# Performance work log

Hardware: AMD Instinct MI355X
Metric: run time of the kernel (lower is better)

## Reference

```python
import jax, jax.numpy as jnp
import numpy as np

N_HEAD, QK_DIM, V_DIM = 8, 32, 32
INNER = N_HEAD * V_DIM  # 256
D_MODEL = 256
N_VAR = 2
NEG = -1e9
LN_EPS = 1e-5


def irregular_rope(q, t):
    # q: [BN, L, H, D], t: [BN, L]
    D = q.shape[-1]
    inv_freq = 1.0 / (10000.0 ** (jnp.arange(0, D, 2, dtype=jnp.float32) / D))  # [D/2]
    ang = t[:, :, None, None] * inv_freq[None, None, None, :]  # [BN, L, 1, D/2]
    cos, sin = jnp.cos(ang), jnp.sin(ang)
    q1, q2 = q[..., 0::2], q[..., 1::2]
    out = jnp.stack([q1 * cos - q2 * sin, q1 * sin + q2 * cos], axis=-1)
    return out.reshape(q.shape)


def layernorm(x, g, b):
    mu = jnp.mean(x, axis=-1, keepdims=True)
    var = jnp.mean((x - mu) ** 2, axis=-1, keepdims=True)
    return (x - mu) * jax.lax.rsqrt(var + LN_EPS) * g + b


def setup_inputs() -> dict:
    key = jax.random.key(0)
    ks = jax.random.split(key, 14)
    B, PN, PL = 16, 64, 128
    x = jax.random.normal(ks[0], (B, PN, PL, N_VAR), dtype=jnp.float32)
    t = jnp.sort(jax.random.uniform(ks[1], (B, PN, PL + 1), dtype=jnp.float32) * 100.0, axis=-1)
    mask = jax.random.randint(ks[2], (B, PN, PL + 1), 0, 2, dtype=jnp.int32)
    mask = mask.at[..., 0].set(1)  # emb token never masked
    s = 0.05
    return {
        "x": x, "t": t, "mask": mask,
        "emb_token": jnp.zeros((1, 1, 1, N_VAR), dtype=jnp.float32),
        "Wq": jax.random.normal(ks[3], (N_VAR, N_HEAD * QK_DIM), dtype=jnp.float32) * s,
        "Wk": jax.random.normal(ks[4], (N_VAR, N_HEAD * QK_DIM), dtype=jnp.float32) * s,
        "Wv": jax.random.normal(ks[5], (N_VAR, N_HEAD * V_DIM), dtype=jnp.float32) * s,
        "Wo": jax.random.normal(ks[6], (INNER, D_MODEL), dtype=jnp.float32) * s,
        "ln_g": jnp.ones((INNER,), dtype=jnp.float32),
        "ln_b": jnp.zeros((INNER,), dtype=jnp.float32),
        "W1": jax.random.normal(ks[7], (INNER, 4 * INNER), dtype=jnp.float32) * s,
        "b1": jnp.zeros((4 * INNER,), dtype=jnp.float32),
        "W2": jax.random.normal(ks[8], (4 * INNER, INNER), dtype=jnp.float32) * s,
        "b2": jnp.zeros((INNER,), dtype=jnp.float32),
    }


def reference(x, t, mask, emb_token, Wq, Wk, Wv, Wo, ln_g, ln_b, W1, b1, W2, b2):
    B, PN, PL, _ = x.shape
    L = PL + 1
    BN = B * PN
    emb = jnp.broadcast_to(emb_token, (B, PN, 1, N_VAR))
    _x = jnp.concatenate([emb, x], axis=2)  # [B, PN, L, 2]
    Q = (_x @ Wq).reshape(BN, L, N_HEAD, QK_DIM)
    K = (_x @ Wk).reshape(BN, L, N_HEAD, QK_DIM)
    V = (_x @ Wv).reshape(BN, L, N_HEAD, V_DIM)
    tt = t.reshape(BN, L)
    Q = irregular_rope(Q, tt)
    K = irregular_rope(K, tt)
    # attention: [BN, H, L, L]
    scores = jnp.einsum('blhd,bmhd->bhlm', Q, K) / jnp.sqrt(jnp.float32(QK_DIM))
    m = mask.reshape(BN, L).astype(jnp.float32)
    mask_mat = (m[:, :, None] * m[:, None, :])[:, None, :, :]  # [BN,1,L,L]
    scores = jnp.where(mask_mat > 0, scores, NEG)
    attn = jax.nn.softmax(scores, axis=-1)
    ctx = jnp.einsum('bhlm,bmhd->blhd', attn, V)  # [BN, L, H, Dv]
    last = ctx[:, 0].reshape(B, PN, INNER)  # emb-token output
    h = layernorm(last, ln_g, ln_b)
    h = jax.nn.relu(h @ W1 + b1) @ W2 + b2
    last = last + h
    return last @ Wo  # [B, PN, D_MODEL]
```

## Files before the change

kernel.cpp:

```cpp
#include <hip/hip_runtime.h>
#include <math.h>

#define LSEQ   129
#define PLEN   128
#define NHEAD  8
#define DHEAD  32
#define INNER  256
#define HID    1024

typedef _Float16 h2 __attribute__((ext_vector_type(2)));

__device__ __forceinline__ float dot2(h2 a, h2 b, float c) {
#if __has_builtin(__builtin_amdgcn_fdot2)
    return __builtin_amdgcn_fdot2(a, b, c, false);
#else
    return c + (float)a.x * (float)b.x + (float)a.y * (float)b.y;
#endif
}

__device__ __forceinline__ h2 pack2(float a, float b) {
    h2 v; v.x = (_Float16)a; v.y = (_Float16)b; return v;
}

__global__ __launch_bounds__(256) void convert_kernel(
    const float* __restrict__ W1, const float* __restrict__ W2,
    const float* __restrict__ Wo,
    h2* __restrict__ W1p, h2* __restrict__ W2p, h2* __restrict__ Wop)
{
    int idx = blockIdx.x * 256 + threadIdx.x;
    if (idx < 131072) {
        int c2 = idx >> 10, jc = idx & 1023;
        W1p[idx] = pack2(W1[(2 * c2) * HID + jc], W1[(2 * c2 + 1) * HID + jc]);
    } else if (idx < 262144) {
        int l = idx - 131072;
        int c2 = l >> 8, jc = l & 255;
        W2p[l] = pack2(W2[(2 * c2) * INNER + jc], W2[(2 * c2 + 1) * INNER + jc]);
    } else if (idx < 294912) {
        int l = idx - 262144;
        int c2 = l >> 8, jc = l & 255;
        Wop[l] = pack2(Wo[(2 * c2) * INNER + jc], Wo[(2 * c2 + 1) * INNER + jc]);
    }
}

__global__ __launch_bounds__(256) void attn_kernel(
    const float* __restrict__ x,
    const float* __restrict__ t,
    const int*   __restrict__ mask,
    const float* __restrict__ emb,
    const float* __restrict__ Wq,
    const float* __restrict__ Wk,
    const float* __restrict__ Wv,
    float*       __restrict__ last)
{
    const int bn  = blockIdx.x;
    const int tid = threadIdx.x;

    __shared__ float2 cs_s[16][132];
    __shared__ float2 x_s[132];
    __shared__ float4 ab_s[8][16];
    __shared__ float  sc_s[8][132];
    __shared__ int    mask_s[132];
    __shared__ float  hstat_s[8][3];

    const float* tb = t + bn * LSEQ;
    const float t0  = tb[0];
    const float e0 = emb[0], e1 = emb[1];

    if (tid < 130) {
        float2 v;
        if (tid == 0)       v = make_float2(e0, e1);
        else if (tid <= 128) v = ((const float2*)(x + bn * PLEN * 2))[tid - 1];
        else                 v = make_float2(0.f, 0.f);
        x_s[tid] = v;
    }
    if (tid < 129) mask_s[tid] = mask[bn * LSEQ + tid];

    for (int i = tid; i < 129 * 16; i += 256) {
        int m = i >> 4, j = i & 15;
        float invf = exp2f(-(float)j * 0.8304820237218407f);
        float sv, cv;
        __sincosf((tb[m] - t0) * invf, &sv, &cv);
        cs_s[j][m] = make_float2(cv, sv);
    }

    if (tid < 128) {
        int h = tid >> 4, j = tid & 15;
        int ce = h * 32 + 2 * j, co = ce + 1;
        float qe = e0 * Wq[ce] + e1 * Wq[256 + ce];
        float qo = e0 * Wq[co] + e1 * Wq[256 + co];
        float k0e = Wk[ce], k0o = Wk[co];
        float k1e = Wk[256 + ce], k1o = Wk[256 + co];
        const float sc = 0.17677669529663687f;
        ab_s[h][j] = make_float4((qe * k0e + qo * k0o) * sc,
                                 (qo * k0e - qe * k0o) * sc,
                                 (qe * k1e + qo * k1o) * sc,
                                 (qo * k1e - qe * k1o) * sc);
    }
    __syncthreads();

    const int lane = tid & 63;
    const int wv   = tid >> 6;
    const int h    = wv * 2 + (lane >> 5);
    const int l32  = lane & 31;

    float4 ab[16];
#pragma unroll
    for (int j = 0; j < 16; ++j) ab[j] = ab_s[h][j];

#pragma unroll
    for (int k = 0; k < 5; ++k) {
        int m = l32 + 32 * k;
        if (m < 129) {
            float2 xv = x_s[m];
            float accA = 0.f, accB = 0.f;
#pragma unroll
            for (int j = 0; j < 16; ++j) {
                float2 cs = cs_s[j][m];
                accA = fmaf(cs.x, ab[j].x, accA);
                accA = fmaf(cs.y, ab[j].y, accA);
                accB = fmaf(cs.x, ab[j].z, accB);
                accB = fmaf(cs.y, ab[j].w, accB);
            }
            sc_s[h][m] = accA * xv.x + accB * xv.y;
        }
    }
    __syncthreads();

    const int mask0 = mask_s[0];
    float se[5];
    float M = -1e30f;
#pragma unroll
    for (int k = 0; k < 5; ++k) {
        int m = l32 + 32 * k;
        float s;
        if (m < 129) {
            s = sc_s[h][m];
            if (mask0 == 0)          s = 0.f;
            else if (mask_s[m] == 0) s = -1e9f;
        } else s = -1e30f;
        se[k] = s;
        M = fmaxf(M, s);
    }
#pragma unroll
    for (int off = 16; off >= 1; off >>= 1) M = fmaxf(M, __shfl_xor(M, off, 64));

    float den = 0.f, S0 = 0.f, S1 = 0.f;
#pragma unroll
    for (int k = 0; k < 5; ++k) {
        int m = l32 + 32 * k;
        if (m < 129) {
            float e = __expf(se[k] - M);
            float2 xv = x_s[m];
            den += e;
            S0 = fmaf(e, xv.x, S0);
            S1 = fmaf(e, xv.y, S1);
        }
    }
#pragma unroll
    for (int off = 16; off >= 1; off >>= 1) {
        den += __shfl_xor(den, off, 64);
        S0  += __shfl_xor(S0,  off, 64);
        S1  += __shfl_xor(S1,  off, 64);
    }
    if (l32 == 0) {
        hstat_s[h][0] = den; hstat_s[h][1] = S0; hstat_s[h][2] = S1;
    }
    __syncthreads();

    {
        int hh = tid >> 5;
        float inv = 1.f / hstat_s[hh][0];
        last[bn * 256 + tid] =
            (hstat_s[hh][1] * Wv[tid] + hstat_s[hh][2] * Wv[256 + tid]) * inv;
    }
}

__global__ __launch_bounds__(1024) void mlp_kernel(
    const float* __restrict__ last,
    const float* __restrict__ ln_g,
    const float* __restrict__ ln_b,
    const h2*    __restrict__ W1p,
    const float* __restrict__ b1,
    const h2*    __restrict__ W2p,
    const float* __restrict__ b2,
    const h2*    __restrict__ Wop,
    float*       __restrict__ out)
{
    const int tid = threadIdx.x;
    const int r0  = blockIdx.x * 4;
    const int rg  = tid >> 8;
    const int ch  = tid & 255;

    __shared__ float x_s[4][INNER];
    __shared__ h2    h2_s[4][128];
    __shared__ h2    y2_s[4][512];
    __shared__ float p_s[4][4][INNER];
    __shared__ h2    r2_s[4][128];
    __shared__ float red_s[16][2];

    float xv = last[(r0 + rg) * INNER + ch];
    x_s[rg][ch] = xv;

    float s1 = xv, s2 = xv * xv;
#pragma unroll
    for (int off = 32; off >= 1; off >>= 1) {
        s1 += __shfl_xor(s1, off, 64);
        s2 += __shfl_xor(s2, off, 64);
    }
    const int wave = tid >> 6;
    if ((tid & 63) == 0) { red_s[wave][0] = s1; red_s[wave][1] = s2; }
    __syncthreads();

    {
        float t1 = red_s[4 * rg + 0][0] + red_s[4 * rg + 1][0] +
                   red_s[4 * rg + 2][0] + red_s[4 * rg + 3][0];
        float t2 = red_s[4 * rg + 0][1] + red_s[4 * rg + 1][1] +
                   red_s[4 * rg + 2][1] + red_s[4 * rg + 3][1];
        float mu  = t1 * (1.f / 256.f);
        float var = t2 * (1.f / 256.f) - mu * mu;
        float rs  = rsqrtf(var + 1e-5f);
        float hv  = (xv - mu) * rs * ln_g[ch] + ln_b[ch];
        float ho  = __shfl_xor(hv, 1, 64);
        if ((ch & 1) == 0) h2_s[rg][ch >> 1] = pack2(hv, ho);
    }
    __syncthreads();

    {
        float a0, a1v, a2v, a3;
        a0 = a1v = a2v = a3 = b1[tid];
        const h2* w = W1p + tid;
#pragma unroll 16
        for (int c2 = 0; c2 < 128; ++c2) {
            h2 wv = w[c2 * HID];
            a0  = dot2(h2_s[0][c2], wv, a0);
            a1v = dot2(h2_s[1][c2], wv, a1v);
            a2v = dot2(h2_s[2][c2], wv, a2v);
            a3  = dot2(h2_s[3][c2], wv, a3);
        }
        a0 = fmaxf(a0, 0.f); a1v = fmaxf(a1v, 0.f);
        a2v = fmaxf(a2v, 0.f); a3 = fmaxf(a3, 0.f);
        float o0 = __shfl_xor(a0, 1, 64);
        float o1 = __shfl_xor(a1v, 1, 64);
        float o2 = __shfl_xor(a2v, 1, 64);
        float o3 = __shfl_xor(a3, 1, 64);
        if ((tid & 1) == 0) {
            int p = tid >> 1;
            y2_s[0][p] = pack2(a0, o0);
            y2_s[1][p] = pack2(a1v, o1);
            y2_s[2][p] = pack2(a2v, o2);
            y2_s[3][p] = pack2(a3, o3);
        }
    }
    __syncthreads();

    {
        float a0 = 0.f, a1v = 0.f, a2v = 0.f, a3 = 0.f;
        const h2* w = W2p + rg * 128 * INNER + ch;
#pragma unroll 16
        for (int i = 0; i < 128; ++i) {
            h2 wv = w[i * INNER];
            int c2 = rg * 128 + i;
            a0  = dot2(y2_s[0][c2], wv, a0);
            a1v = dot2(y2_s[1][c2], wv, a1v);
            a2v = dot2(y2_s[2][c2], wv, a2v);
            a3  = dot2(y2_s[3][c2], wv, a3);
        }
        p_s[rg][0][ch] = a0;
        p_s[rg][1][ch] = a1v;
        p_s[rg][2][ch] = a2v;
        p_s[rg][3][ch] = a3;
    }
    __syncthreads();

    {
        float rv = x_s[rg][ch] + b2[ch] +
                   p_s[0][rg][ch] + p_s[1][rg][ch] +
                   p_s[2][rg][ch] + p_s[3][rg][ch];
        float ro = __shfl_xor(rv, 1, 64);
        if ((ch & 1) == 0) r2_s[rg][ch >> 1] = pack2(rv, ro);
    }
    __syncthreads();

    {
        float a0 = 0.f, a1v = 0.f, a2v = 0.f, a3 = 0.f;
        const h2* w = Wop + rg * 32 * INNER + ch;
#pragma unroll
        for (int i = 0; i < 32; ++i) {
            h2 wv = w[i * INNER];
            int c2 = rg * 32 + i;
            a0  = dot2(r2_s[0][c2], wv, a0);
            a1v = dot2(r2_s[1][c2], wv, a1v);
            a2v = dot2(r2_s[2][c2], wv, a2v);
            a3  = dot2(r2_s[3][c2], wv, a3);
        }
        p_s[rg][0][ch] = a0;
        p_s[rg][1][ch] = a1v;
        p_s[rg][2][ch] = a2v;
        p_s[rg][3][ch] = a3;
    }
    __syncthreads();

    out[(r0 + rg) * INNER + ch] = p_s[0][rg][ch] + p_s[1][rg][ch] +
                                  p_s[2][rg][ch] + p_s[3][rg][ch];
}

extern "C" void kernel_launch(void* const* d_in, const int* in_sizes, int n_in,
                              void* d_out, int out_size, void* d_ws, size_t ws_size,
                              hipStream_t stream) {
    const float* x    = (const float*)d_in[0];
    const float* t    = (const float*)d_in[1];
    const int*   mask = (const int*)  d_in[2];
    const float* emb  = (const float*)d_in[3];
    const float* Wq   = (const float*)d_in[4];
    const float* Wk   = (const float*)d_in[5];
    const float* Wv   = (const float*)d_in[6];
    const float* Wo   = (const float*)d_in[7];
    const float* ln_g = (const float*)d_in[8];
    const float* ln_b = (const float*)d_in[9];
    const float* W1   = (const float*)d_in[10];
    const float* b1   = (const float*)d_in[11];
    const float* W2   = (const float*)d_in[12];
    const float* b2   = (const float*)d_in[13];
    float* out = (float*)d_out;

    const int BN = in_sizes[1] / LSEQ;

    char* ws = (char*)d_ws;
    float* last_ws = (float*)ws;
    h2* W1p = (h2*)(ws + (1u << 20));
    h2* W2p = (h2*)(ws + (1u << 20) + (512u << 10));
    h2* Wop = (h2*)(ws + (2u << 20));

    convert_kernel<<<1152, 256, 0, stream>>>(W1, W2, Wo, W1p, W2p, Wop);
    attn_kernel<<<BN, 256, 0, stream>>>(x, t, mask, emb, Wq, Wk, Wv, last_ws);
    mlp_kernel<<<BN / 4, 1024, 0, stream>>>(last_ws, ln_g, ln_b, W1p, b1,
                                            W2p, b2, Wop, out);
}
```

Measured before the change: 111.8 us.

## Fuse weight fp16 conversion into attention kernel and use 8-wide packed weights

Removes the separate convert kernel launch by having each attention block convert a slice of W1/W2/Wo to fp16 before its attention work. The packed format changes from pairs to groups of 8 halves, so the MLP kernel issues 128-bit weight loads and 128-bit LDS reads with four dot2 ops each, instead of 32-bit loads. Activations are stored as plain fp16 arrays in shared memory without the shuffle-based pairing. The fused conversion adds a strided global read prologue to every attention block. Correctness relies on the attention kernel finishing before the MLP kernel starts, which stream ordering guarantees.

Result: faster. 108.0 us (-3.4%).

```diff
diff --git a/kernel.cpp b/kernel.cpp
--- a/kernel.cpp
+++ b/kernel.cpp
@@ -9,8 +9,9 @@
 #define HID    1024
 
 typedef _Float16 h2 __attribute__((ext_vector_type(2)));
-
-__device__ __forceinline__ float dot2(h2 a, h2 b, float c) {
+typedef _Float16 h8 __attribute__((ext_vector_type(8)));
+
+__device__ __forceinline__ float fdot2(h2 a, h2 b, float c) {
 #if __has_builtin(__builtin_amdgcn_fdot2)
     return __builtin_amdgcn_fdot2(a, b, c, false);
 #else
@@ -18,28 +19,20 @@
 #endif
 }
 
-__device__ __forceinline__ h2 pack2(float a, float b) {
-    h2 v; v.x = (_Float16)a; v.y = (_Float16)b; return v;
-}
-
-__global__ __launch_bounds__(256) void convert_kernel(
-    const float* __restrict__ W1, const float* __restrict__ W2,
-    const float* __restrict__ Wo,
-    h2* __restrict__ W1p, h2* __restrict__ W2p, h2* __restrict__ Wop)
-{
-    int idx = blockIdx.x * 256 + threadIdx.x;
-    if (idx < 131072) {
-        int c2 = idx >> 10, jc = idx & 1023;
-        W1p[idx] = pack2(W1[(2 * c2) * HID + jc], W1[(2 * c2 + 1) * HID + jc]);
-    } else if (idx < 262144) {
-        int l = idx - 131072;
-        int c2 = l >> 8, jc = l & 255;
-        W2p[l] = pack2(W2[(2 * c2) * INNER + jc], W2[(2 * c2 + 1) * INNER + jc]);
-    } else if (idx < 294912) {
-        int l = idx - 262144;
-        int c2 = l >> 8, jc = l & 255;
-        Wop[l] = pack2(Wo[(2 * c2) * INNER + jc], Wo[(2 * c2 + 1) * INNER + jc]);
-    }
+__device__ __forceinline__ float dot8(h8 a, h8 b, float c) {
+    h2 a0 = __builtin_shufflevector(a, a, 0, 1);
+    h2 a1 = __builtin_shufflevector(a, a, 2, 3);
+    h2 a2 = __builtin_shufflevector(a, a, 4, 5);
+    h2 a3 = __builtin_shufflevector(a, a, 6, 7);
+    h2 b0 = __builtin_shufflevector(b, b, 0, 1);
+    h2 b1 = __builtin_shufflevector(b, b, 2, 3);
+    h2 b2 = __builtin_shufflevector(b, b, 4, 5);
+    h2 b3 = __builtin_shufflevector(b, b, 6, 7);
+    c = fdot2(a0, b0, c);
+    c = fdot2(a1, b1, c);
+    c = fdot2(a2, b2, c);
+    c = fdot2(a3, b3, c);
+    return c;
 }
 
 __global__ __launch_bounds__(256) void attn_kernel(
@@ -50,10 +43,44 @@
     const float* __restrict__ Wq,
     const float* __restrict__ Wk,
     const float* __restrict__ Wv,
-    float*       __restrict__ last)
+    const float* __restrict__ W1,
+    const float* __restrict__ W2,
+    const float* __restrict__ Wo,
+    float*       __restrict__ last,
+    h8*          __restrict__ W1o,
+    h8*          __restrict__ W2o,
+    h8*          __restrict__ Woo)
 {
     const int bn  = blockIdx.x;
     const int tid = threadIdx.x;
+
+    {
+        int g = bn * 256 + tid;
+        if (g < 73728) {
+            h8 v;
+            if (g < 32768) {
+                int c8 = g >> 10, j = g & 1023;
+                const float* src = W1 + (8 * c8) * HID + j;
+#pragma unroll
+                for (int i = 0; i < 8; ++i) v[i] = (_Float16)src[i * HID];
+                W1o[g] = v;
+            } else if (g < 65536) {
+                int l = g - 32768;
+                int c8 = l >> 8, o = l & 255;
+                const float* src = W2 + (8 * c8) * INNER + o;
+#pragma unroll
+                for (int i = 0; i < 8; ++i) v[i] = (_Float16)src[i * INNER];
+                W2o[l] = v;
+            } else {
+                int l = g - 65536;
+                int c8 = l >> 8, o = l & 255;
+                const float* src = Wo + (8 * c8) * INNER + o;
+#pragma unroll
+                for (int i = 0; i < 8; ++i) v[i] = (_Float16)src[i * INNER];
+                Woo[l] = v;
+            }
+        }
+    }
 
     __shared__ float2 cs_s[16][132];
     __shared__ float2 x_s[132];
@@ -68,7 +95,7 @@
 
     if (tid < 130) {
         float2 v;
-        if (tid == 0)       v = make_float2(e0, e1);
+        if (tid == 0)        v = make_float2(e0, e1);
         else if (tid <= 128) v = ((const float2*)(x + bn * PLEN * 2))[tid - 1];
         else                 v = make_float2(0.f, 0.f);
         x_s[tid] = v;
@@ -179,11 +206,11 @@
     const float* __restrict__ last,
     const float* __restrict__ ln_g,
     const float* __restrict__ ln_b,
-    const h2*    __restrict__ W1p,
+    const h8*    __restrict__ W1o,
     const float* __restrict__ b1,
-    const h2*    __restrict__ W2p,
+    const h8*    __restrict__ W2o,
     const float* __restrict__ b2,
-    const h2*    __restrict__ Wop,
+    const h8*    __restrict__ Woo,
     float*       __restrict__ out)
 {
     const int tid = threadIdx.x;
@@ -192,10 +219,10 @@
     const int ch  = tid & 255;
 
     __shared__ float x_s[4][INNER];
-    __shared__ h2    h2_s[4][128];
-    __shared__ h2    y2_s[4][512];
+    __shared__ alignas(16) _Float16 h_h[4][INNER];
+    __shared__ alignas(16) _Float16 y_h[4][HID];
+    __shared__ alignas(16) _Float16 r_h[4][INNER];
     __shared__ float p_s[4][4][INNER];
-    __shared__ h2    r2_s[4][128];
     __shared__ float red_s[16][2];
 
     float xv = last[(r0 + rg) * INNER + ch];
@@ -219,51 +246,48 @@
         float mu  = t1 * (1.f / 256.f);
         float var = t2 * (1.f / 256.f) - mu * mu;
         float rs  = rsqrtf(var + 1e-5f);
-        float hv  = (xv - mu) * rs * ln_g[ch] + ln_b[ch];
-        float ho  = __shfl_xor(hv, 1, 64);
-        if ((ch & 1) == 0) h2_s[rg][ch >> 1] = pack2(hv, ho);
+        h_h[rg][ch] = (_Float16)((xv - mu) * rs * ln_g[ch] + ln_b[ch]);
     }
     __syncthreads();
 
     {
         float a0, a1v, a2v, a3;
         a0 = a1v = a2v = a3 = b1[tid];
-        const h2* w = W1p + tid;
-#pragma unroll 16
-        for (int c2 = 0; c2 < 128; ++c2) {
-            h2 wv = w[c2 * HID];
-            a0  = dot2(h2_s[0][c2], wv, a0);
-            a1v = dot2(h2_s[1][c2], wv, a1v);
-            a2v = dot2(h2_s[2][c2], wv, a2v);
-            a3  = dot2(h2_s[3][c2], wv, a3);
-        }
-        a0 = fmaxf(a0, 0.f); a1v = fmaxf(a1v, 0.f);
-        a2v = fmaxf(a2v, 0.f); a3 = fmaxf(a3, 0.f);
-        float o0 = __shfl_xor(a0, 1, 64);
-        float o1 = __shfl_xor(a1v, 1, 64);
-        float o2 = __shfl_xor(a2v, 1, 64);
-        float o3 = __shfl_xor(a3, 1, 64);
-        if ((tid & 1) == 0) {
-            int p = tid >> 1;
-            y2_s[0][p] = pack2(a0, o0);
-            y2_s[1][p] = pack2(a1v, o1);
-            y2_s[2][p] = pack2(a2v, o2);
-            y2_s[3][p] = pack2(a3, o3);
-        }
+        const h8* w = W1o + tid;
+#pragma unroll 8
+        for (int c8 = 0; c8 < 32; ++c8) {
+            h8 wv = w[c8 * HID];
+            h8 h0 = *(const h8*)&h_h[0][c8 * 8];
+            h8 h1 = *(const h8*)&h_h[1][c8 * 8];
+            h8 hh2 = *(const h8*)&h_h[2][c8 * 8];
+            h8 h3 = *(const h8*)&h_h[3][c8 * 8];
+            a0  = dot8(h0, wv, a0);
+            a1v = dot8(h1, wv, a1v);
+            a2v = dot8(hh2, wv, a2v);
+            a3  = dot8(h3, wv, a3);
+        }
+        y_h[0][tid] = (_Float16)fmaxf(a0, 0.f);
+        y_h[1][tid] = (_Float16)fmaxf(a1v, 0.f);
+        y_h[2][tid] = (_Float16)fmaxf(a2v, 0.f);
+        y_h[3][tid] = (_Float16)fmaxf(a3, 0.f);
     }
     __syncthreads();
 
     {
         float a0 = 0.f, a1v = 0.f, a2v = 0.f, a3 = 0.f;
-        const h2* w = W2p + rg * 128 * INNER + ch;
-#pragma unroll 16
-        for (int i = 0; i < 128; ++i) {
-            h2 wv = w[i * INNER];
-            int c2 = rg * 128 + i;
-            a0  = dot2(y2_s[0][c2], wv, a0);
-            a1v = dot2(y2_s[1][c2], wv, a1v);
-            a2v = dot2(y2_s[2][c2], wv, a2v);
-            a3  = dot2(y2_s[3][c2], wv, a3);
+        const h8* w = W2o + rg * 32 * INNER + ch;
+#pragma unroll 8
+        for (int i = 0; i < 32; ++i) {
+            int c8 = rg * 32 + i;
+            h8 wv = w[i * INNER];
+            h8 y0 = *(const h8*)&y_h[0][c8 * 8];
+            h8 y1 = *(const h8*)&y_h[1][c8 * 8];
+            h8 y2 = *(const h8*)&y_h[2][c8 * 8];
+            h8 y3 = *(const h8*)&y_h[3][c8 * 8];
+            a0  = dot8(y0, wv, a0);
+            a1v = dot8(y1, wv, a1v);
+            a2v = dot8(y2, wv, a2v);
+            a3  = dot8(y3, wv, a3);
         }
         p_s[rg][0][ch] = a0;
         p_s[rg][1][ch] = a1v;
@@ -276,22 +300,25 @@
         float rv = x_s[rg][ch] + b2[ch] +
                    p_s[0][rg][ch] + p_s[1][rg][ch] +
                    p_s[2][rg][ch] + p_s[3][rg][ch];
-        float ro = __shfl_xor(rv, 1, 64);
-        if ((ch & 1) == 0) r2_s[rg][ch >> 1] = pack2(rv, ro);
+        r_h[rg][ch] = (_Float16)rv;
     }
     __syncthreads();
 
     {
         float a0 = 0.f, a1v = 0.f, a2v = 0.f, a3 = 0.f;
-        const h2* w = Wop + rg * 32 * INNER + ch;
-#pragma unroll
-        for (int i = 0; i < 32; ++i) {
-            h2 wv = w[i * INNER];
-            int c2 = rg * 32 + i;
-            a0  = dot2(r2_s[0][c2], wv, a0);
-            a1v = dot2(r2_s[1][c2], wv, a1v);
-            a2v = dot2(r2_s[2][c2], wv, a2v);
-            a3  = dot2(r2_s[3][c2], wv, a3);
+        const h8* w = Woo + rg * 8 * INNER + ch;
+#pragma unroll
+        for (int i = 0; i < 8; ++i) {
+            int c8 = rg * 8 + i;
+            h8 wv = w[i * INNER];
+            h8 v0 = *(const h8*)&r_h[0][c8 * 8];
+            h8 v1 = *(const h8*)&r_h[1][c8 * 8];
+            h8 v2 = *(const h8*)&r_h[2][c8 * 8];
+            h8 v3 = *(const h8*)&r_h[3][c8 * 8];
+            a0  = dot8(v0, wv, a0);
+            a1v = dot8(v1, wv, a1v);
+            a2v = dot8(v2, wv, a2v);
+            a3  = dot8(v3, wv, a3);
         }
         p_s[rg][0][ch] = a0;
         p_s[rg][1][ch] = a1v;
@@ -327,12 +354,12 @@
 
     char* ws = (char*)d_ws;
     float* last_ws = (float*)ws;
-    h2* W1p = (h2*)(ws + (1u << 20));
-    h2* W2p = (h2*)(ws + (1u << 20) + (512u << 10));
-    h2* Wop = (h2*)(ws + (2u << 20));
-
-    convert_kernel<<<1152, 256, 0, stream>>>(W1, W2, Wo, W1p, W2p, Wop);
-    attn_kernel<<<BN, 256, 0, stream>>>(x, t, mask, emb, Wq, Wk, Wv, last_ws);
-    mlp_kernel<<<BN / 4, 1024, 0, stream>>>(last_ws, ln_g, ln_b, W1p, b1,
-                                            W2p, b2, Wop, out);
-}
+    h8* W1o = (h8*)(ws + (1u << 20));
+    h8* W2o = (h8*)(ws + (1u << 20) + (512u << 10));
+    h8* Woo = (h8*)(ws + (2u << 20));
+
+    attn_kernel<<<BN, 256, 0, stream>>>(x, t, mask, emb, Wq, Wk, Wv,
+                                        W1, W2, Wo, last_ws, W1o, W2o, Woo);
+    mlp_kernel<<<BN / 4, 1024, 0, stream>>>(last_ws, ln_g, ln_b, W1o, b1,
+                                            W2o, b2, Woo, out);
+}
```
